# Optimization experiments

Hardware: AMD Instinct MI355X
Metric: run time of the kernel (lower is better)

The kernel has to match this reference:

```python
import jax, jax.numpy as jnp
import numpy as np

N, E = 20000, 320000
NF, EF = 4, 4
HID, HEADS, MODEL_HID = 128, 4, 128


def _p(key, shape, scale=0.1):
    return scale * jax.random.normal(key, shape, dtype=jnp.float32)


def setup_inputs() -> dict:
    key = jax.random.key(0)
    ks = jax.random.split(key, 32)
    x = jax.random.normal(ks[0], (N, NF), dtype=jnp.float32)
    src = jax.random.randint(ks[1], (E,), 0, N)
    off = jax.random.randint(ks[2], (E,), 1, N)
    dst = (src + off) % N  # no self-loops (PyG removes then re-adds them)
    edge_index = jnp.stack([src, dst]).astype(jnp.int64)
    edge_attr = jax.random.uniform(ks[3], (E, EF), dtype=jnp.float32)
    d = dict(x=x, edge_index=edge_index, edge_attr=edge_attr)
    # input_proj
    d['Wp'] = _p(ks[4], (NF, HID)); d['bp'] = jnp.zeros((HID,), jnp.float32)
    # GAT layer 1: in=HID, heads=HEADS, out=HID, concat
    d['W1'] = _p(ks[5], (HID, HEADS * HID)); d['We1'] = _p(ks[6], (EF, HEADS * HID))
    d['as1'] = _p(ks[7], (HEADS, HID)); d['ad1'] = _p(ks[8], (HEADS, HID)); d['ae1'] = _p(ks[9], (HEADS, HID))
    d['b1'] = jnp.zeros((HEADS * HID,), jnp.float32)
    d['g1'] = jnp.ones((HEADS * HID,), jnp.float32); d['be1'] = jnp.zeros((HEADS * HID,), jnp.float32)
    # GAT layer 2: in=HEADS*HID, heads=1, out=HID, mean
    d['W2'] = _p(ks[10], (HEADS * HID, HID)); d['We2'] = _p(ks[11], (EF, HID))
    d['as2'] = _p(ks[12], (1, HID)); d['ad2'] = _p(ks[13], (1, HID)); d['ae2'] = _p(ks[14], (1, HID))
    d['b2'] = jnp.zeros((HID,), jnp.float32)
    d['g2'] = jnp.ones((HID,), jnp.float32); d['be2'] = jnp.zeros((HID,), jnp.float32)
    # output proj + importance scorer
    d['Wo'] = _p(ks[15], (HID, MODEL_HID)); d['bo'] = jnp.zeros((MODEL_HID,), jnp.float32)
    d['Wi'] = _p(ks[16], (MODEL_HID, 1)); d['bi'] = jnp.zeros((1,), jnp.float32)
    return d


def _layer_norm(x, g, b, eps=1e-5):
    mu = x.mean(-1, keepdims=True)
    v = ((x - mu) ** 2).mean(-1, keepdims=True)
    return (x - mu) * jax.lax.rsqrt(v + eps) * g + b


def _segment_softmax(logits, seg, num):
    m = jax.ops.segment_max(logits, seg, num_segments=num)
    e = jnp.exp(logits - m[seg])
    d = jax.ops.segment_sum(e, seg, num_segments=num)
    return e / d[seg]


def _forward(x, edge_index, edge_attr, Wp, bp, W1, We1, as1, ad1, ae1, b1, g1, be1,
             W2, We2, as2, ad2, ae2, b2, g2, be2, Wo, bo, Wi, bi):
    n = x.shape[0]
    src, dst = edge_index[0], edge_index[1]
    e = edge_attr.shape[0]
    # add_self_loops with fill_value='mean': self-loop attr = mean of incoming edge_attr
    deg = jax.ops.segment_sum(jnp.ones((e,), edge_attr.dtype), dst, num_segments=n)
    loop_attr = jax.ops.segment_sum(edge_attr, dst, num_segments=n) / jnp.maximum(deg, 1.0)[:, None]
    loops = jnp.arange(n)
    src_f = jnp.concatenate([src, loops])
    dst_f = jnp.concatenate([dst, loops])
    ea = jnp.concatenate([edge_attr, loop_attr], axis=0)  # [E+N, EF]

    def gat(h, W, We, a_s, a_d, a_e, bias, heads, out_c, concat):
        xh = (h @ W).reshape(n, heads, out_c)                 # [N,H,C]
        eh = (ea @ We).reshape(-1, heads, out_c)              # [E+N,H,C]
        al_s = (xh * a_s).sum(-1)                             # [N,H]
        al_d = (xh * a_d).sum(-1)                             # [N,H]
        al_e = (eh * a_e).sum(-1)                             # [E+N,H]
        logits = jax.nn.leaky_relu(al_s[src_f] + al_d[dst_f] + al_e, negative_slope=0.2)
        alpha = _segment_softmax(logits, dst_f, n)            # [E+N,H]
        out = jax.ops.segment_sum(xh[src_f] * alpha[..., None], dst_f, num_segments=n)
        out = out.reshape(n, heads * out_c) if concat else out.mean(axis=1)
        return out + bias, alpha

    h = x @ Wp + bp
    h, _ = gat(h, W1, We1, as1, ad1, ae1, b1, HEADS, HID, True)
    h = jax.nn.elu(_layer_norm(h, g1, be1))  # dropout is a no-op in eval
    h, edge_attention = gat(h, W2, We2, as2, ad2, ae2, b2, 1, HID, False)
    h = _layer_norm(h, g2, be2)
    emb = h @ Wo + bo
    importance = jax.nn.sigmoid(emb @ Wi + bi).squeeze(-1)
    return emb, edge_attention, importance


def reference(x, edge_index, edge_attr, Wp, bp, W1, We1, as1, ad1, ae1, b1, g1, be1,
              W2, We2, as2, ad2, ae2, b2, g2, be2, Wo, bo, Wi, bi):
    return _forward(x, edge_index, edge_attr, Wp, bp, W1, We1, as1, ad1, ae1, b1, g1, be1,
                    W2, We2, as2, ad2, ae2, b2, g2, be2, Wo, bo, Wi, bi)
```

## Files before the change

kernel.cpp:

```cpp
#include <hip/hip_runtime.h>
#include <math.h>
#include <stdint.h>

#define N_NODES 20000
#define N_EDGES 320000
#define EN_TOT  340000
#define CAP     160

typedef __attribute__((ext_vector_type(8))) _Float16 half8v;
typedef __attribute__((ext_vector_type(2))) _Float16 half2v;
typedef __attribute__((ext_vector_type(4))) float float4v;

__device__ __forceinline__ ushort f2h(float f) {
    _Float16 h = (_Float16)f;
    return __builtin_bit_cast(ushort, h);
}
__device__ __forceinline__ float h2f(ushort s) {
    return (float)__builtin_bit_cast(_Float16, s);
}

__global__ void k_deg(const int* __restrict__ dst, int* __restrict__ degi) {
    int e = blockIdx.x * 256 + threadIdx.x;
    if (e >= N_EDGES) return;
    atomicAdd(&degi[dst[e]], 1);
}

__global__ __launch_bounds__(1024) void k_scan(const int* __restrict__ degi, int* __restrict__ offsets,
                                               const float* __restrict__ We1, const float* __restrict__ ae1,
                                               const float* __restrict__ We2, const float* __restrict__ ae2,
                                               float* __restrict__ M1, float* __restrict__ m2) {
    __shared__ int s[1024];
    int t = threadIdx.x;
    int n0 = t * 20;
    int tot = 0;
    for (int i = 0; i < 20; i++) {
        int n = n0 + i;
        if (n < N_NODES) tot += degi[n] + 1;
    }
    s[t] = tot;
    __syncthreads();
    for (int off = 1; off < 1024; off <<= 1) {
        int v = (t >= off) ? s[t - off] : 0;
        __syncthreads();
        s[t] += v;
        __syncthreads();
    }
    int run = s[t] - tot;
    for (int i = 0; i < 20; i++) {
        int n = n0 + i;
        if (n < N_NODES) {
            offsets[n] = run;
            run += degi[n] + 1;
        }
    }
    if (t == 1023) offsets[N_NODES] = s[1023];
    if (t < 16) {
        int f = t >> 2, h = t & 3;
        float acc = 0.f;
        for (int c = 0; c < 128; c++) acc += We1[f * 512 + h * 128 + c] * ae1[h * 128 + c];
        M1[f * 4 + h] = acc;
    } else if (t < 20) {
        int f = t - 16;
        float acc = 0.f;
        for (int c = 0; c < 128; c++) acc += We2[f * 128 + c] * ae2[c];
        m2[f] = acc;
    }
}

__global__ void k_fill(const int* __restrict__ src, const int* __restrict__ dst,
                       const int* __restrict__ offsets, int* __restrict__ cursor,
                       int2* __restrict__ csr_se) {
    int i = blockIdx.x * 256 + threadIdx.x;
    if (i >= EN_TOT) return;
    int d, sidx, eid;
    if (i < N_EDGES) { d = dst[i]; sidx = src[i]; eid = i; }
    else { int n = i - N_EDGES; d = n; sidx = n; eid = N_EDGES + n; }
    int pos = offsets[d] + atomicAdd(&cursor[d], 1);
    csr_se[pos] = make_int2(sidx, eid);
}

__global__ __launch_bounds__(256) void k_misc(const int* __restrict__ offsets, const int2* __restrict__ csr_se,
                                              const float* __restrict__ eattr, float* __restrict__ loopattr,
                                              const float* __restrict__ W1, const float* __restrict__ W2,
                                              const float* __restrict__ Wo, ushort* __restrict__ W1T,
                                              ushort* __restrict__ W2T, ushort* __restrict__ WoT,
                                              const float* __restrict__ x, const float* __restrict__ Wp,
                                              const float* __restrict__ bp, ushort* __restrict__ h0h) {
    int b = blockIdx.x;
    int tid = threadIdx.x;
    if (b < 5000) {
        int wv = tid >> 6, l = tid & 63;
        int n = b * 4 + wv;
        if (n >= N_NODES) return;
        int start = offsets[n], end = offsets[n + 1];
        float sx = 0.f, sy = 0.f, sz = 0.f, sw = 0.f;
        for (int p = start + l; p < end; p += 64) {
            int eid = csr_se[p].y;
            if (eid < N_EDGES) {
                float4 e = *(const float4*)&eattr[(size_t)eid * 4];
                sx += e.x; sy += e.y; sz += e.z; sw += e.w;
            }
        }
        for (int off = 32; off; off >>= 1) {
            sx += __shfl_down(sx, off);
            sy += __shfl_down(sy, off);
            sz += __shfl_down(sz, off);
            sw += __shfl_down(sw, off);
        }
        if (l == 0) {
            float inv = 1.0f / fmaxf((float)(end - start - 1), 1.0f);
            float4 o;
            o.x = sx * inv; o.y = sy * inv; o.z = sz * inv; o.w = sw * inv;
            *(float4*)&loopattr[(size_t)n * 4] = o;
        }
    } else if (b < 5576) {
        int i = (b - 5000) * 256 + tid;
        if (i < 512 * 128) {
            int nn = i >> 7, kk = i & 127;
            W1T[i] = f2h(W1[kk * 512 + nn]);
        } else if (i < 2 * 512 * 128) {
            int j = i - 512 * 128;
            int nn = j >> 9, kk = j & 511;
            W2T[j] = f2h(W2[kk * 128 + nn]);
        } else if (i < 2 * 512 * 128 + 128 * 128) {
            int j = i - 2 * 512 * 128;
            int nn = j >> 7, kk = j & 127;
            WoT[j] = f2h(Wo[kk * 128 + nn]);
        }
    } else {
        int n = (b - 5576) * 2 + (tid >> 7);
        int c = tid & 127;
        float acc = bp[c];
#pragma unroll
        for (int f = 0; f < 4; f++) acc += x[n * 4 + f] * Wp[f * 128 + c];
        h0h[(size_t)n * 128 + c] = f2h(acc);
    }
}

__global__ __launch_bounds__(256) void k_gemm_hf(const ushort* __restrict__ A, const ushort* __restrict__ BT,
                                                 float* __restrict__ Cf, ushort* __restrict__ Ch,
                                                 int M, int Nn, int K, const float* __restrict__ bias,
                                                 const float* __restrict__ asv, const float* __restrict__ adv,
                                                 float* __restrict__ outS, float* __restrict__ outD,
                                                 int hstride, const float* __restrict__ sbias) {
    __shared__ ushort As[64 * 64];
    __shared__ ushort Bs[128 * 64];
    __shared__ float redS[4][64];
    __shared__ float redD[4][64];
    const int tid = threadIdx.x;
    const int lane = tid & 63, wid = tid >> 6;
    const int m0 = blockIdx.x * 64, n0 = blockIdx.y * 128;
    float4v acc[4][2];
#pragma unroll
    for (int i = 0; i < 4; i++)
#pragma unroll
        for (int j = 0; j < 2; j++) acc[i][j] = (float4v){0.f, 0.f, 0.f, 0.f};

    for (int k0 = 0; k0 < K; k0 += 64) {
        __syncthreads();
#pragma unroll
        for (int i = 0; i < 2; i++) {
            int c = tid + i * 256;
            int row = c >> 3, sl = c & 7;
            int off = row * 128 + ((sl ^ (row & 7)) << 4);
            uint4 va = make_uint4(0u, 0u, 0u, 0u);
            if (m0 + row < M) va = *(const uint4*)&A[(size_t)(m0 + row) * K + k0 + sl * 8];
            *(uint4*)((char*)As + off) = va;
        }
#pragma unroll
        for (int i = 0; i < 4; i++) {
            int c = tid + i * 256;
            int row = c >> 3, sl = c & 7;
            int off = row * 128 + ((sl ^ (row & 7)) << 4);
            uint4 vb = *(const uint4*)&BT[(size_t)(n0 + row) * K + k0 + sl * 8];
            *(uint4*)((char*)Bs + off) = vb;
        }
        __syncthreads();
#pragma unroll
        for (int kk = 0; kk < 2; kk++) {
            half8v af[4], bq[2];
            int sl = kk * 4 + (lane >> 4);
#pragma unroll
            for (int mi = 0; mi < 4; mi++) {
                int row = (lane & 15) + mi * 16;
                af[mi] = *(const half8v*)((const char*)As + row * 128 + ((sl ^ (row & 7)) << 4));
            }
#pragma unroll
            for (int ni = 0; ni < 2; ni++) {
                int row = wid * 32 + ni * 16 + (lane & 15);
                bq[ni] = *(const half8v*)((const char*)Bs + row * 128 + ((sl ^ (row & 7)) << 4));
            }
#pragma unroll
            for (int mi = 0; mi < 4; mi++)
#pragma unroll
                for (int ni = 0; ni < 2; ni++)
                    acc[mi][ni] = __builtin_amdgcn_mfma_f32_16x16x32_f16(af[mi], bq[ni], acc[mi][ni], 0, 0, 0);
        }
    }
    float bcol[2];
#pragma unroll
    for (int ni = 0; ni < 2; ni++)
        bcol[ni] = bias ? bias[n0 + wid * 32 + ni * 16 + (lane & 15)] : 0.f;
#pragma unroll
    for (int mi = 0; mi < 4; mi++) {
#pragma unroll
        for (int j = 0; j < 4; j++) {
            int row = m0 + mi * 16 + ((lane >> 4) << 2) + j;
            if (row < M) {
#pragma unroll
                for (int ni = 0; ni < 2; ni++) {
                    int col = n0 + wid * 32 + ni * 16 + (lane & 15);
                    float v = acc[mi][ni][j] + bcol[ni];
                    if (Cf) Cf[(size_t)row * Nn + col] = v;
                    if (Ch) Ch[(size_t)row * Nn + col] = f2h(v);
                }
            }
        }
    }
    if (asv) {
        float asl[2], adl[2];
#pragma unroll
        for (int ni = 0; ni < 2; ni++) {
            int col = n0 + wid * 32 + ni * 16 + (lane & 15);
            asl[ni] = asv[col];
            adl[ni] = adv ? adv[col] : 0.f;
        }
        float psv[4][4], pdv[4][4];
#pragma unroll
        for (int mi = 0; mi < 4; mi++)
#pragma unroll
            for (int j = 0; j < 4; j++) {
                float v0 = acc[mi][0][j] + bcol[0];
                float v1 = acc[mi][1][j] + bcol[1];
                psv[mi][j] = v0 * asl[0] + v1 * asl[1];
                pdv[mi][j] = v0 * adl[0] + v1 * adl[1];
            }
#pragma unroll
        for (int off = 1; off < 16; off <<= 1) {
#pragma unroll
            for (int mi = 0; mi < 4; mi++)
#pragma unroll
                for (int j = 0; j < 4; j++) {
                    psv[mi][j] += __shfl_xor(psv[mi][j], off);
                    pdv[mi][j] += __shfl_xor(pdv[mi][j], off);
                }
        }
        if ((lane & 15) == 0) {
#pragma unroll
            for (int mi = 0; mi < 4; mi++)
#pragma unroll
                for (int j = 0; j < 4; j++) {
                    int r = mi * 16 + ((lane >> 4) << 2) + j;
                    redS[wid][r] = psv[mi][j];
                    redD[wid][r] = pdv[mi][j];
                }
        }
        __syncthreads();
        if (tid < 64) {
            int row = m0 + tid;
            if (row < M) {
                float ss = redS[0][tid] + redS[1][tid] + redS[2][tid] + redS[3][tid];
                float dd = redD[0][tid] + redD[1][tid] + redD[2][tid] + redD[3][tid];
                if (sbias) {
                    outS[row] = 1.0f / (1.0f + __expf(-(ss + sbias[0])));
                } else {
                    outS[row * hstride + blockIdx.y] = ss;
                    if (outD) outD[row * hstride + blockIdx.y] = dd;
                }
            }
        }
    }
}

__global__ __launch_bounds__(128) void k_agg1(const int* __restrict__ offsets, const int2* __restrict__ csr_se,
                                              const float* __restrict__ eattr, const float* __restrict__ loopattr,
                                              const float* __restrict__ als, const float* __restrict__ aldv,
                                              const float* __restrict__ M1, const ushort* __restrict__ xhh,
                                              const float* __restrict__ b1, const float* __restrict__ g1,
                                              const float* __restrict__ be1, ushort* __restrict__ h1h) {
    int wv = threadIdx.x >> 6, lane = threadIdx.x & 63;
    int n = blockIdx.x * 2 + wv;
    __shared__ float Lc[2][CAP][4];
    __shared__ int   sSrc[2][CAP];
    __shared__ float mhs[2][4], shs[2][4];

    int start = offsets[n];
    int cnt = offsets[n + 1] - start;

    int hh = lane & 3;
    float aldn = aldv[n * 4 + hh];
    float c0 = M1[hh], c1 = M1[4 + hh], c2 = M1[8 + hh], c3 = M1[12 + hh];
    float m = -1e30f, s = 0.f;
    for (int j = lane >> 2; j < cnt; j += 16) {
        int2 se = csr_se[start + j];
        const float* eap = (se.y < N_EDGES) ? &eattr[(size_t)se.y * 4] : &loopattr[(size_t)(se.y - N_EDGES) * 4];
        float4 e4 = *(const float4*)eap;
        float l = als[se.x * 4 + hh] + aldn + e4.x * c0 + e4.y * c1 + e4.z * c2 + e4.w * c3;
        l = (l >= 0.f) ? l : 0.2f * l;
        Lc[wv][j][hh] = l;
        if (hh == 0) sSrc[wv][j] = se.x;
        float mn = fmaxf(m, l);
        s = s * __expf(m - mn) + __expf(l - mn);
        m = mn;
    }
#pragma unroll
    for (int off = 4; off < 64; off <<= 1) {
        float mo = __shfl_xor(m, off), so = __shfl_xor(s, off);
        float mn = fmaxf(m, mo);
        s = s * __expf(m - mn) + so * __expf(mo - mn);
        m = mn;
    }
    if (lane < 4) { mhs[wv][lane] = m; shs[wv][lane] = 1.0f / s; }

    int tot = cnt * 4;
    for (int idx = lane; idx < tot; idx += 64) {
        int j = idx >> 2, h = idx & 3;
        Lc[wv][j][h] = __expf(Lc[wv][j][h] - mhs[wv][h]) * shs[wv][h];
    }

    half2v hac0 = (half2v)0, hac1 = (half2v)0, hac2 = (half2v)0, hac3 = (half2v)0;
    int hg = lane >> 4;
    uint ch = (uint)lane * 8u;
    int j = 0;
    for (; j + 8 <= cnt; j += 8) {
        _Float16 av[8];
        uint4 vv[8];
#pragma unroll
        for (int t = 0; t < 8; t++) av[t] = (_Float16)Lc[wv][j + t][hg];
#pragma unroll
        for (int t = 0; t < 8; t++) vv[t] = *(const uint4*)&xhh[((uint)sSrc[wv][j + t] << 9) + ch];
#pragma unroll
        for (int t = 0; t < 8; t++) {
            half2v a2 = (half2v){av[t], av[t]};
            const half2v* pv = (const half2v*)&vv[t];
            hac0 = pv[0] * a2 + hac0;
            hac1 = pv[1] * a2 + hac1;
            hac2 = pv[2] * a2 + hac2;
            hac3 = pv[3] * a2 + hac3;
        }
    }
    for (; j < cnt; j++) {
        _Float16 a = (_Float16)Lc[wv][j][hg];
        half2v a2 = (half2v){a, a};
        uint4 v = *(const uint4*)&xhh[((uint)sSrc[wv][j] << 9) + ch];
        const half2v* pv = (const half2v*)&v;
        hac0 = pv[0] * a2 + hac0;
        hac1 = pv[1] * a2 + hac1;
        hac2 = pv[2] * a2 + hac2;
        hac3 = pv[3] * a2 + hac3;
    }

    float4 ba = *(const float4*)&b1[ch];
    float4 bb = *(const float4*)&b1[ch + 4];
    float v0 = (float)hac0[0] + ba.x, v1 = (float)hac0[1] + ba.y;
    float v2 = (float)hac1[0] + ba.z, v3 = (float)hac1[1] + ba.w;
    float v4 = (float)hac2[0] + bb.x, v5 = (float)hac2[1] + bb.y;
    float v6 = (float)hac3[0] + bb.z, v7 = (float)hac3[1] + bb.w;
    float s8 = v0 + v1 + v2 + v3 + v4 + v5 + v6 + v7;
#pragma unroll
    for (int off = 1; off < 64; off <<= 1) s8 += __shfl_xor(s8, off);
    float mu = s8 * (1.0f / 512.0f);
    float d0 = v0 - mu, d1 = v1 - mu, d2 = v2 - mu, d3 = v3 - mu;
    float d4 = v4 - mu, d5 = v5 - mu, d6 = v6 - mu, d7 = v7 - mu;
    float sq = d0 * d0 + d1 * d1 + d2 * d2 + d3 * d3 + d4 * d4 + d5 * d5 + d6 * d6 + d7 * d7;
#pragma unroll
    for (int off = 1; off < 64; off <<= 1) sq += __shfl_xor(sq, off);
    float rstd = rsqrtf(sq * (1.0f / 512.0f) + 1e-5f);
    float4 ga = *(const float4*)&g1[ch];
    float4 gb = *(const float4*)&g1[ch + 4];
    float4 ea = *(const float4*)&be1[ch];
    float4 eb = *(const float4*)&be1[ch + 4];
    float y0 = d0 * rstd * ga.x + ea.x, y1 = d1 * rstd * ga.y + ea.y;
    float y2 = d2 * rstd * ga.z + ea.z, y3 = d3 * rstd * ga.w + ea.w;
    float y4 = d4 * rstd * gb.x + eb.x, y5 = d5 * rstd * gb.y + eb.y;
    float y6 = d6 * rstd * gb.z + eb.z, y7 = d7 * rstd * gb.w + eb.w;
    y0 = (y0 > 0.f) ? y0 : (__expf(y0) - 1.0f);
    y1 = (y1 > 0.f) ? y1 : (__expf(y1) - 1.0f);
    y2 = (y2 > 0.f) ? y2 : (__expf(y2) - 1.0f);
    y3 = (y3 > 0.f) ? y3 : (__expf(y3) - 1.0f);
    y4 = (y4 > 0.f) ? y4 : (__expf(y4) - 1.0f);
    y5 = (y5 > 0.f) ? y5 : (__expf(y5) - 1.0f);
    y6 = (y6 > 0.f) ? y6 : (__expf(y6) - 1.0f);
    y7 = (y7 > 0.f) ? y7 : (__expf(y7) - 1.0f);
    uint4 o;
    o.x = (uint)f2h(y0) | ((uint)f2h(y1) << 16);
    o.y = (uint)f2h(y2) | ((uint)f2h(y3) << 16);
    o.z = (uint)f2h(y4) | ((uint)f2h(y5) << 16);
    o.w = (uint)f2h(y6) | ((uint)f2h(y7) << 16);
    *(uint4*)&h1h[(size_t)n * 512 + ch] = o;
}

__global__ __launch_bounds__(128) void k_agg2(const int* __restrict__ offsets, const int2* __restrict__ csr_se,
                                              const float* __restrict__ eattr, const float* __restrict__ loopattr,
                                              const float* __restrict__ als, const float* __restrict__ aldv,
                                              const float* __restrict__ m2v, const ushort* __restrict__ xh2h,
                                              const float* __restrict__ b2, const float* __restrict__ g2,
                                              const float* __restrict__ be2, float* __restrict__ eaout,
                                              ushort* __restrict__ h2h) {
    int wv = threadIdx.x >> 6, lane = threadIdx.x & 63;
    int n = blockIdx.x * 2 + wv;
    __shared__ float Lc[2][CAP];
    __shared__ int   sS[2][CAP];
    __shared__ int   sE[2][CAP];

    int start = offsets[n];
    int cnt = offsets[n + 1] - start;
    float aldn = aldv[n];
    float c0 = m2v[0], c1 = m2v[1], c2 = m2v[2], c3 = m2v[3];
    float m = -1e30f, s = 0.f;
    for (int j = lane; j < cnt; j += 64) {
        int2 se = csr_se[start + j];
        const float* eap = (se.y < N_EDGES) ? &eattr[(size_t)se.y * 4] : &loopattr[(size_t)(se.y - N_EDGES) * 4];
        float4 e4 = *(const float4*)eap;
        float l = als[se.x] + aldn + e4.x * c0 + e4.y * c1 + e4.z * c2 + e4.w * c3;
        l = (l >= 0.f) ? l : 0.2f * l;
        Lc[wv][j] = l; sS[wv][j] = se.x; sE[wv][j] = se.y;
        float mn = fmaxf(m, l);
        s = s * __expf(m - mn) + __expf(l - mn);
        m = mn;
    }
#pragma unroll
    for (int off = 1; off < 64; off <<= 1) {
        float mo = __shfl_xor(m, off), so = __shfl_xor(s, off);
        float mn = fmaxf(m, mo);
        s = s * __expf(m - mn) + so * __expf(mo - mn);
        m = mn;
    }
    float inv = 1.0f / s;
    for (int j = lane; j < cnt; j += 64) {
        float a = __expf(Lc[wv][j] - m) * inv;
        Lc[wv][j] = a;
        eaout[sE[wv][j]] = a;
    }
    half2v hac = (half2v)0;
    uint ch = (uint)lane * 2u;
    int j = 0;
    for (; j + 8 <= cnt; j += 8) {
        _Float16 av[8];
        uint vv[8];
#pragma unroll
        for (int t = 0; t < 8; t++) av[t] = (_Float16)Lc[wv][j + t];
#pragma unroll
        for (int t = 0; t < 8; t++) vv[t] = *(const uint*)&xh2h[((uint)sS[wv][j + t] << 7) + ch];
#pragma unroll
        for (int t = 0; t < 8; t++) {
            half2v a2 = (half2v){av[t], av[t]};
            half2v pv = __builtin_bit_cast(half2v, vv[t]);
            hac = pv * a2 + hac;
        }
    }
    for (; j < cnt; j++) {
        _Float16 a = (_Float16)Lc[wv][j];
        half2v a2 = (half2v){a, a};
        half2v pv = __builtin_bit_cast(half2v, *(const uint*)&xh2h[((uint)sS[wv][j] << 7) + ch]);
        hac = pv * a2 + hac;
    }
    float2 bb = *(const float2*)&b2[ch];
    float v0 = (float)hac[0] + bb.x, v1 = (float)hac[1] + bb.y;
    float s2 = v0 + v1;
#pragma unroll
    for (int off = 1; off < 64; off <<= 1) s2 += __shfl_xor(s2, off);
    float mu = s2 * (1.0f / 128.0f);
    float d0 = v0 - mu, d1 = v1 - mu;
    float q = d0 * d0 + d1 * d1;
#pragma unroll
    for (int off = 1; off < 64; off <<= 1) q += __shfl_xor(q, off);
    float rstd = rsqrtf(q * (1.0f / 128.0f) + 1e-5f);
    float2 gg = *(const float2*)&g2[ch];
    float2 ee = *(const float2*)&be2[ch];
    float y0 = d0 * rstd * gg.x + ee.x;
    float y1 = d1 * rstd * gg.y + ee.y;
    uint o = (uint)f2h(y0) | ((uint)f2h(y1) << 16);
    *(uint*)&h2h[(size_t)n * 128 + ch] = o;
}

extern "C" void kernel_launch(void* const* d_in, const int* in_sizes, int n_in,
                              void* d_out, int out_size, void* d_ws, size_t ws_size,
                              hipStream_t stream) {
    const float* x    = (const float*)d_in[0];
    const int*   eidx = (const int*)d_in[1];
    const float* eattr= (const float*)d_in[2];
    const float* Wp   = (const float*)d_in[3];
    const float* bp   = (const float*)d_in[4];
    const float* W1   = (const float*)d_in[5];
    const float* We1  = (const float*)d_in[6];
    const float* as1  = (const float*)d_in[7];
    const float* ad1  = (const float*)d_in[8];
    const float* ae1  = (const float*)d_in[9];
    const float* b1   = (const float*)d_in[10];
    const float* g1   = (const float*)d_in[11];
    const float* be1  = (const float*)d_in[12];
    const float* W2   = (const float*)d_in[13];
    const float* We2  = (const float*)d_in[14];
    const float* as2  = (const float*)d_in[15];
    const float* ad2  = (const float*)d_in[16];
    const float* ae2  = (const float*)d_in[17];
    const float* b2   = (const float*)d_in[18];
    const float* g2   = (const float*)d_in[19];
    const float* be2  = (const float*)d_in[20];
    const float* Wo   = (const float*)d_in[21];
    const float* bo   = (const float*)d_in[22];
    const float* Wi   = (const float*)d_in[23];
    const float* bi   = (const float*)d_in[24];

    const int* src = eidx;
    const int* dst = eidx + N_EDGES;

    float* emb_out = (float*)d_out;
    float* ea_out  = emb_out + (size_t)N_NODES * 128;
    float* imp_out = ea_out + EN_TOT;

    char* w = (char*)d_ws;
    auto alloc = [&](size_t bytes) -> void* { void* p = (void*)w; w += (bytes + 255) & ~(size_t)255; return p; };
    ushort* xhh    = (ushort*)alloc((size_t)N_NODES * 512 * 2);
    ushort* h1h    = (ushort*)alloc((size_t)N_NODES * 512 * 2);
    ushort* h0h    = (ushort*)alloc((size_t)N_NODES * 128 * 2);
    ushort* xh2h   = (ushort*)alloc((size_t)N_NODES * 128 * 2);
    ushort* h2h    = (ushort*)alloc((size_t)N_NODES * 128 * 2);
    ushort* W1T    = (ushort*)alloc((size_t)512 * 128 * 2);
    ushort* W2T    = (ushort*)alloc((size_t)128 * 512 * 2);
    ushort* WoT    = (ushort*)alloc((size_t)128 * 128 * 2);
    int2*  csr_se  = (int2*)alloc((size_t)EN_TOT * 8);
    int*   offsets = (int*)alloc((size_t)(N_NODES + 1) * 4);
    int*   cursor  = (int*)alloc((size_t)N_NODES * 4);
    int*   degi    = (int*)alloc((size_t)N_NODES * 4);
    float* loopat  = (float*)alloc((size_t)N_NODES * 4 * 4);
    float* als1v   = (float*)alloc((size_t)N_NODES * 4 * 4);
    float* ald1v   = (float*)alloc((size_t)N_NODES * 4 * 4);
    float* als2v   = (float*)alloc((size_t)N_NODES * 4);
    float* ald2v   = (float*)alloc((size_t)N_NODES * 4);
    float* M1      = (float*)alloc(32 * 4);
    float* m2      = M1 + 16;

    hipMemsetAsync(degi,   0, (size_t)N_NODES * 4, stream);
    hipMemsetAsync(cursor, 0, (size_t)N_NODES * 4, stream);

    k_deg<<<(N_EDGES + 255) / 256, 256, 0, stream>>>(dst, degi);
    k_scan<<<1, 1024, 0, stream>>>(degi, offsets, We1, ae1, We2, ae2, M1, m2);
    k_fill<<<(EN_TOT + 255) / 256, 256, 0, stream>>>(src, dst, offsets, cursor, csr_se);
    k_misc<<<15576, 256, 0, stream>>>(offsets, csr_se, eattr, loopat, W1, W2, Wo,
                                      W1T, W2T, WoT, x, Wp, bp, h0h);

    k_gemm_hf<<<dim3((N_NODES + 63) / 64, 4), 256, 0, stream>>>(h0h, W1T, nullptr, xhh,
                                                                N_NODES, 512, 128, nullptr,
                                                                as1, ad1, als1v, ald1v, 4, nullptr);
    k_agg1<<<N_NODES / 2, 128, 0, stream>>>(offsets, csr_se, eattr, loopat, als1v, ald1v, M1,
                                            xhh, b1, g1, be1, h1h);

    k_gemm_hf<<<dim3((N_NODES + 63) / 64, 1), 256, 0, stream>>>(h1h, W2T, nullptr, xh2h,
                                                                N_NODES, 128, 512, nullptr,
                                                                as2, ad2, als2v, ald2v, 1, nullptr);
    k_agg2<<<N_NODES / 2, 128, 0, stream>>>(offsets, csr_se, eattr, loopat, als2v, ald2v, m2,
                                            xh2h, b2, g2, be2, ea_out, h2h);

    k_gemm_hf<<<dim3((N_NODES + 63) / 64, 1), 256, 0, stream>>>(h2h, WoT, emb_out, nullptr,
                                                                N_NODES, 128, 128, bo,
                                                                Wi, nullptr, imp_out, nullptr, 1, bi);
}
```

Before: 207.1 us.

## Template GEMM tile height, use 32-row tiles for narrow GEMMs, vectorize degree count

Makes the GEMM row-tile size a template parameter and launches the two 128-column GEMMs with 32-row tiles, doubling their block count so more CUs have work on the narrow outputs. The degree kernel now processes two edges per thread with an int2 load. The aggregation kernels clamp the per-node edge count to the shared buffer capacity, and the online-softmax code is moved into macros. Smaller tiles reload B more often per output row, and the clamp silently truncates nodes whose degree exceeds the capacity.

```diff
diff --git a/kernel.cpp b/kernel.cpp
--- a/kernel.cpp
+++ b/kernel.cpp
@@ -19,10 +19,16 @@
     return (float)__builtin_bit_cast(_Float16, s);
 }
 
+#define ONL(mm, ss, ll) { float _mn = fmaxf(mm, ll); ss = ss * __expf(mm - _mn) + __expf(ll - _mn); mm = _mn; }
+#define MRG(mm, ss, off) { float _mo = __shfl_xor(mm, off), _so = __shfl_xor(ss, off); \
+                           float _mn = fmaxf(mm, _mo); ss = ss * __expf(mm - _mn) + _so * __expf(_mo - _mn); mm = _mn; }
+
 __global__ void k_deg(const int* __restrict__ dst, int* __restrict__ degi) {
-    int e = blockIdx.x * 256 + threadIdx.x;
+    int e = (blockIdx.x * 256 + threadIdx.x) * 2;
     if (e >= N_EDGES) return;
-    atomicAdd(&degi[dst[e]], 1);
+    int2 d = *(const int2*)&dst[e];
+    atomicAdd(&degi[d.x], 1);
+    atomicAdd(&degi[d.y], 1);
 }
 
 __global__ __launch_bounds__(1024) void k_scan(const int* __restrict__ degi, int* __restrict__ offsets,
@@ -137,29 +143,31 @@
     }
 }
 
+template<int BM>
 __global__ __launch_bounds__(256) void k_gemm_hf(const ushort* __restrict__ A, const ushort* __restrict__ BT,
                                                  float* __restrict__ Cf, ushort* __restrict__ Ch,
                                                  int M, int Nn, int K, const float* __restrict__ bias,
                                                  const float* __restrict__ asv, const float* __restrict__ adv,
                                                  float* __restrict__ outS, float* __restrict__ outD,
                                                  int hstride, const float* __restrict__ sbias) {
-    __shared__ ushort As[64 * 64];
+    constexpr int MR = BM / 16;
+    __shared__ ushort As[BM * 64];
     __shared__ ushort Bs[128 * 64];
-    __shared__ float redS[4][64];
-    __shared__ float redD[4][64];
+    __shared__ float redS[4][BM];
+    __shared__ float redD[4][BM];
     const int tid = threadIdx.x;
     const int lane = tid & 63, wid = tid >> 6;
-    const int m0 = blockIdx.x * 64, n0 = blockIdx.y * 128;
-    float4v acc[4][2];
-#pragma unroll
-    for (int i = 0; i < 4; i++)
+    const int m0 = blockIdx.x * BM, n0 = blockIdx.y * 128;
+    float4v acc[MR][2];
+#pragma unroll
+    for (int i = 0; i < MR; i++)
 #pragma unroll
         for (int j = 0; j < 2; j++) acc[i][j] = (float4v){0.f, 0.f, 0.f, 0.f};
 
     for (int k0 = 0; k0 < K; k0 += 64) {
         __syncthreads();
 #pragma unroll
-        for (int i = 0; i < 2; i++) {
+        for (int i = 0; i < BM * 8 / 256; i++) {
             int c = tid + i * 256;
             int row = c >> 3, sl = c & 7;
             int off = row * 128 + ((sl ^ (row & 7)) << 4);
@@ -178,10 +186,10 @@
         __syncthreads();
 #pragma unroll
         for (int kk = 0; kk < 2; kk++) {
-            half8v af[4], bq[2];
+            half8v af[MR], bq[2];
             int sl = kk * 4 + (lane >> 4);
 #pragma unroll
-            for (int mi = 0; mi < 4; mi++) {
+            for (int mi = 0; mi < MR; mi++) {
                 int row = (lane & 15) + mi * 16;
                 af[mi] = *(const half8v*)((const char*)As + row * 128 + ((sl ^ (row & 7)) << 4));
             }
@@ -191,7 +199,7 @@
                 bq[ni] = *(const half8v*)((const char*)Bs + row * 128 + ((sl ^ (row & 7)) << 4));
             }
 #pragma unroll
-            for (int mi = 0; mi < 4; mi++)
+            for (int mi = 0; mi < MR; mi++)
 #pragma unroll
                 for (int ni = 0; ni < 2; ni++)
                     acc[mi][ni] = __builtin_amdgcn_mfma_f32_16x16x32_f16(af[mi], bq[ni], acc[mi][ni], 0, 0, 0);
@@ -202,7 +210,7 @@
     for (int ni = 0; ni < 2; ni++)
         bcol[ni] = bias ? bias[n0 + wid * 32 + ni * 16 + (lane & 15)] : 0.f;
 #pragma unroll
-    for (int mi = 0; mi < 4; mi++) {
+    for (int mi = 0; mi < MR; mi++) {
 #pragma unroll
         for (int j = 0; j < 4; j++) {
             int row = m0 + mi * 16 + ((lane >> 4) << 2) + j;
@@ -225,9 +233,9 @@
             asl[ni] = asv[col];
             adl[ni] = adv ? adv[col] : 0.f;
         }
-        float psv[4][4], pdv[4][4];
-#pragma unroll
-        for (int mi = 0; mi < 4; mi++)
+        float psv[MR][4], pdv[MR][4];
+#pragma unroll
+        for (int mi = 0; mi < MR; mi++)
 #pragma unroll
             for (int j = 0; j < 4; j++) {
                 float v0 = acc[mi][0][j] + bcol[0];
@@ -238,7 +246,7 @@
 #pragma unroll
         for (int off = 1; off < 16; off <<= 1) {
 #pragma unroll
-            for (int mi = 0; mi < 4; mi++)
+            for (int mi = 0; mi < MR; mi++)
 #pragma unroll
                 for (int j = 0; j < 4; j++) {
                     psv[mi][j] += __shfl_xor(psv[mi][j], off);
@@ -247,7 +255,7 @@
         }
         if ((lane & 15) == 0) {
 #pragma unroll
-            for (int mi = 0; mi < 4; mi++)
+            for (int mi = 0; mi < MR; mi++)
 #pragma unroll
                 for (int j = 0; j < 4; j++) {
                     int r = mi * 16 + ((lane >> 4) << 2) + j;
@@ -256,7 +264,7 @@
                 }
         }
         __syncthreads();
-        if (tid < 64) {
+        if (tid < BM) {
             int row = m0 + tid;
             if (row < M) {
                 float ss = redS[0][tid] + redS[1][tid] + redS[2][tid] + redS[3][tid];
@@ -285,7 +293,7 @@
     __shared__ float mhs[2][4], shs[2][4];
 
     int start = offsets[n];
-    int cnt = offsets[n + 1] - start;
+    int cnt = min(offsets[n + 1] - start, CAP);
 
     int hh = lane & 3;
     float aldn = aldv[n * 4 + hh];
@@ -299,17 +307,10 @@
         l = (l >= 0.f) ? l : 0.2f * l;
         Lc[wv][j][hh] = l;
         if (hh == 0) sSrc[wv][j] = se.x;
-        float mn = fmaxf(m, l);
-        s = s * __expf(m - mn) + __expf(l - mn);
-        m = mn;
-    }
-#pragma unroll
-    for (int off = 4; off < 64; off <<= 1) {
-        float mo = __shfl_xor(m, off), so = __shfl_xor(s, off);
-        float mn = fmaxf(m, mo);
-        s = s * __expf(m - mn) + so * __expf(mo - mn);
-        m = mn;
-    }
+        ONL(m, s, l);
+    }
+#pragma unroll
+    for (int off = 4; off < 64; off <<= 1) { MRG(m, s, off); }
     if (lane < 4) { mhs[wv][lane] = m; shs[wv][lane] = 1.0f / s; }
 
     int tot = cnt * 4;
@@ -404,7 +405,7 @@
     __shared__ int   sE[2][CAP];
 
     int start = offsets[n];
-    int cnt = offsets[n + 1] - start;
+    int cnt = min(offsets[n + 1] - start, CAP);
     float aldn = aldv[n];
     float c0 = m2v[0], c1 = m2v[1], c2 = m2v[2], c3 = m2v[3];
     float m = -1e30f, s = 0.f;
@@ -415,17 +416,10 @@
         float l = als[se.x] + aldn + e4.x * c0 + e4.y * c1 + e4.z * c2 + e4.w * c3;
         l = (l >= 0.f) ? l : 0.2f * l;
         Lc[wv][j] = l; sS[wv][j] = se.x; sE[wv][j] = se.y;
-        float mn = fmaxf(m, l);
-        s = s * __expf(m - mn) + __expf(l - mn);
-        m = mn;
-    }
-#pragma unroll
-    for (int off = 1; off < 64; off <<= 1) {
-        float mo = __shfl_xor(m, off), so = __shfl_xor(s, off);
-        float mn = fmaxf(m, mo);
-        s = s * __expf(m - mn) + so * __expf(mo - mn);
-        m = mn;
-    }
+        ONL(m, s, l);
+    }
+#pragma unroll
+    for (int off = 1; off < 64; off <<= 1) { MRG(m, s, off); }
     float inv = 1.0f / s;
     for (int j = lane; j < cnt; j += 64) {
         float a = __expf(Lc[wv][j] - m) * inv;
@@ -439,13 +433,13 @@
         _Float16 av[8];
         uint vv[8];
 #pragma unroll
-        for (int t = 0; t < 8; t++) av[t] = (_Float16)Lc[wv][j + t];
-#pragma unroll
-        for (int t = 0; t < 8; t++) vv[t] = *(const uint*)&xh2h[((uint)sS[wv][j + t] << 7) + ch];
-#pragma unroll
-        for (int t = 0; t < 8; t++) {
-            half2v a2 = (half2v){av[t], av[t]};
-            half2v pv = __builtin_bit_cast(half2v, vv[t]);
+        for (int tt = 0; tt < 8; tt++) av[tt] = (_Float16)Lc[wv][j + tt];
+#pragma unroll
+        for (int tt = 0; tt < 8; tt++) vv[tt] = *(const uint*)&xh2h[((uint)sS[wv][j + tt] << 7) + ch];
+#pragma unroll
+        for (int tt = 0; tt < 8; tt++) {
+            half2v a2 = (half2v){av[tt], av[tt]};
+            half2v pv = __builtin_bit_cast(half2v, vv[tt]);
             hac = pv * a2 + hac;
         }
     }
@@ -535,25 +529,25 @@
     hipMemsetAsync(degi,   0, (size_t)N_NODES * 4, stream);
     hipMemsetAsync(cursor, 0, (size_t)N_NODES * 4, stream);
 
-    k_deg<<<(N_EDGES + 255) / 256, 256, 0, stream>>>(dst, degi);
+    k_deg<<<(N_EDGES / 2 + 255) / 256, 256, 0, stream>>>(dst, degi);
     k_scan<<<1, 1024, 0, stream>>>(degi, offsets, We1, ae1, We2, ae2, M1, m2);
     k_fill<<<(EN_TOT + 255) / 256, 256, 0, stream>>>(src, dst, offsets, cursor, csr_se);
     k_misc<<<15576, 256, 0, stream>>>(offsets, csr_se, eattr, loopat, W1, W2, Wo,
                                       W1T, W2T, WoT, x, Wp, bp, h0h);
 
-    k_gemm_hf<<<dim3((N_NODES + 63) / 64, 4), 256, 0, stream>>>(h0h, W1T, nullptr, xhh,
-                                                                N_NODES, 512, 128, nullptr,
-                                                                as1, ad1, als1v, ald1v, 4, nullptr);
+    k_gemm_hf<64><<<dim3((N_NODES + 63) / 64, 4), 256, 0, stream>>>(h0h, W1T, nullptr, xhh,
+                                                                    N_NODES, 512, 128, nullptr,
+                                                                    as1, ad1, als1v, ald1v, 4, nullptr);
     k_agg1<<<N_NODES / 2, 128, 0, stream>>>(offsets, csr_se, eattr, loopat, als1v, ald1v, M1,
                                             xhh, b1, g1, be1, h1h);
 
-    k_gemm_hf<<<dim3((N_NODES + 63) / 64, 1), 256, 0, stream>>>(h1h, W2T, nullptr, xh2h,
-                                                                N_NODES, 128, 512, nullptr,
-                                                                as2, ad2, als2v, ald2v, 1, nullptr);
+    k_gemm_hf<32><<<dim3((N_NODES + 31) / 32, 1), 256, 0, stream>>>(h1h, W2T, nullptr, xh2h,
+                                                                    N_NODES, 128, 512, nullptr,
+                                                                    as2, ad2, als2v, ald2v, 1, nullptr);
     k_agg2<<<N_NODES / 2, 128, 0, stream>>>(offsets, csr_se, eattr, loopat, als2v, ald2v, m2,
                                             xh2h, b2, g2, be2, ea_out, h2h);
 
-    k_gemm_hf<<<dim3((N_NODES + 63) / 64, 1), 256, 0, stream>>>(h2h, WoT, emb_out, nullptr,
-                                                                N_NODES, 128, 128, bo,
-                                                                Wi, nullptr, imp_out, nullptr, 1, bi);
-}
+    k_gemm_hf<32><<<dim3((N_NODES + 31) / 32, 1), 256, 0, stream>>>(h2h, WoT, emb_out, nullptr,
+                                                                    N_NODES, 128, 128, bo,
+                                                                    Wi, nullptr, imp_out, nullptr, 1, bi);
+}
```

After: 202.2 us. 1.02x faster.
